# Kernel tuning notes

Hardware: AMD Instinct MI355X
Metric: run time of the kernel (lower is better)

The kernel has to match this reference:

```python
import jax, jax.numpy as jnp
import numpy as np
from jax import lax

B, NR, NT, M, NUM_ITER = 16384, 64, 32, 4, 64


def setup_inputs() -> dict:
    key = jax.random.key(0)
    k1, k2, k3 = jax.random.split(key, 3)
    yt = jax.random.normal(k1, (B, NR), dtype=jnp.float32)
    # scale channel to keep the 64-step unrolled descent numerically stable
    Ht = 0.1 * jax.random.normal(k2, (B, NR, NT), dtype=jnp.float32)
    sigmat0 = 0.5 + 0.5 * jax.random.uniform(k3, (B,), dtype=jnp.float32)
    m = jnp.array([-3.0, -1.0, 1.0, 3.0], dtype=jnp.float32)          # 4-PAM constellation
    alpha = jnp.full((M,), 0.25, dtype=jnp.float32)                    # uniform prior
    taui = jnp.ones((NUM_ITER + 1,), dtype=jnp.float32)                # taui0 = 1
    delta = jnp.full((NUM_ITER,), 0.1, dtype=jnp.float32)              # delta0 = 0.1
    return {"yt": yt, "Ht": Ht, "sigmat0": sigmat0, "m": m, "alpha": alpha,
            "taui": taui, "delta": delta}


def reference(yt, Ht, sigmat0, m, alpha, taui, delta):
    # Precompute as in CMDNet.call
    HH = jnp.einsum('bri,brj->bij', Ht, Ht)          # [B, Nt, Nt] = H^T H
    yH = jnp.einsum('br,brj->bj', yt, Ht)            # [B, Nt]     = y^T H
    Bsz, _, Nt = Ht.shape
    Mc = m.shape[0]
    n_iter = delta.shape[0]

    G0 = jnp.zeros((Bsz, Nt, Mc), dtype=Ht.dtype)
    sig2 = (sigmat0 ** 2)[:, None, None]             # [B,1,1]
    log_alpha = jnp.log(alpha)                       # [M]
    taui_abs = jnp.abs(taui)                         # [num_iter+1]
    # first layer uses scale 1 in the softmax (first_iter=True), but taui_abs in grad_x
    ft_scale = taui_abs[:n_iter].at[0].set(1.0)

    def step(G, inp):
        scale, ta, d = inp
        ft = jax.nn.softmax((log_alpha + G) * scale, axis=-1)   # [B,Nt,M]
        xt = jnp.sum(ft * m, axis=-1)                           # [B,Nt] soft symbol
        xHH = jnp.einsum('bi,bij->bj', xt, HH)                  # [B,Nt]
        grad_x = ta * (ft * m - ft * xt[..., None])             # [B,Nt,M]
        grad_L = sig2 * (1.0 - jnp.exp(-G)) + grad_x * (xHH - yH)[..., None]
        return G - d * grad_L, None

    G, _ = lax.scan(step, G0, (ft_scale, taui_abs[:n_iter], delta))

    # last layer (last_iter=True): softmax + soft symbol only, no update
    ft = jax.nn.softmax((log_alpha + G) * taui_abs[n_iter], axis=-1)
    xt = jnp.sum(ft * m, axis=-1)
    return ft, xt
```

## Files before the change

kernel.cpp:

```cpp
#include <hip/hip_runtime.h>


#define NRr 64
#define NTt 32
#define NITER 64
#define B_TOTAL 16384

using f16x8  = __attribute__((ext_vector_type(8))) _Float16;
using h16x2  = __attribute__((ext_vector_type(2))) _Float16;
using f32x16 = __attribute__((ext_vector_type(16))) float;

static __device__ __forceinline__ uint32_t pk16(float a, float b) {
    union { _Float16 h[2]; uint32_t u; } x;
    x.h[0] = (_Float16)a; x.h[1] = (_Float16)b;
    return x.u;
}

static __device__ __forceinline__ float fdot2u(uint32_t a, uint32_t b, float c) {
    union { uint32_t u; h16x2 h; } x, y;
    x.u = a; y.u = b;
#if __has_builtin(__builtin_amdgcn_fdot2)
    return __builtin_amdgcn_fdot2(x.h, y.h, c, false);
#else
    return c + (float)x.h[0] * (float)y.h[0] + (float)x.h[1] * (float)y.h[1];
#endif
}

static __device__ __forceinline__ float exp2fast(float x) {
#if __has_builtin(__builtin_amdgcn_exp2f)
    return __builtin_amdgcn_exp2f(x);
#else
    return exp2f(x);
#endif
}

static __device__ __forceinline__ float rdlane(float v, int lane) {
    return __builtin_bit_cast(float,
        __builtin_amdgcn_readlane(__builtin_bit_cast(int, v), lane));
}

static __device__ __forceinline__ float rfl(float v) {
    return __builtin_bit_cast(float,
        __builtin_amdgcn_readfirstlane(__builtin_bit_cast(int, v)));
}

static __device__ __forceinline__ void gram_one(
    const float* __restrict__ hp, const float* __restrict__ ypt,
    const int hi, uint32_t ap[8], float& ypart_out)
{
    f32x16 acc = {};
    float  ypart = 0.f;
#pragma unroll
    for (int kc = 0; kc < 4; ++kc) {
        const int kb = kc * 16 + hi * 8;
        float h[8];
#pragma unroll
        for (int e = 0; e < 8; ++e) h[e] = hp[(size_t)(kb + e) * NTt];
        const float4 ya = *(const float4*)(ypt + kb);
        const float4 yb = *(const float4*)(ypt + kb + 4);
        ypart += h[0]*ya.x + h[1]*ya.y + h[2]*ya.z + h[3]*ya.w
               + h[4]*yb.x + h[5]*yb.y + h[6]*yb.z + h[7]*yb.w;
        f16x8 fa;
#pragma unroll
        for (int e = 0; e < 8; ++e) fa[e] = (_Float16)h[e];
        acc = __builtin_amdgcn_mfma_f32_32x32x16_f16(fa, fa, acc, 0, 0, 0);
    }
#pragma unroll
    for (int g = 0; g < 4; ++g) {
        ap[2*g+0] = pk16(acc[4*g+0], acc[4*g+1]);
        ap[2*g+1] = pk16(acc[4*g+2], acc[4*g+3]);
    }
    ypart_out = ypart;
}

static __device__ __forceinline__ void exch_hh(
    const uint32_t apx[8], const uint32_t apy[8], const int hi, uint32_t hh[16])
{
#pragma unroll
    for (int p = 0; p < 8; ++p) {
        const uint32_t snd = hi ? apx[p] : apy[p];
        const uint32_t rcv = (uint32_t)__shfl_xor((int)snd, 32, 64);
        const uint32_t own = hi ? apy[p] : apx[p];
        const int g = p >> 1, cc = p & 1;
        hh[4*g + cc]     = hi ? rcv : own;
        hh[4*g + 2 + cc] = hi ? own : rcv;
    }
}

__global__ __launch_bounds__(256)
__attribute__((amdgpu_waves_per_eu(4, 4)))
void cmdnet_kernel(
    const float* __restrict__ yt,
    const float* __restrict__ Ht,
    const float* __restrict__ sig0,
    const float* __restrict__ mm,
    const float* __restrict__ alpha,
    const float* __restrict__ taui,
    const float* __restrict__ delta,
    float* __restrict__ out)
{
    __shared__ __align__(16) _Float16 xtsh[4][4][32];

    const int tid = threadIdx.x;
    const int w   = tid >> 6;
    const int l   = tid & 63;
    const int j   = l & 31;
    const int hi  = l >> 5;
    const int c0  = (blockIdx.x * 4 + w) * 4;

    const float vta = fabsf(taui[l]);
    const float vd  = delta[l];

    const size_t hstride = (size_t)NRr * NTt;

    uint32_t hhA[16], hhB[16];
    float yHA_v, yHB_v;
    {
        uint32_t apx[8], apy[8];
        float ypx, ypy;
        gram_one(Ht + (size_t)(c0    ) * hstride + j, yt + (size_t)(c0    ) * NRr, hi, apx, ypx);
        gram_one(Ht + (size_t)(c0 + 2) * hstride + j, yt + (size_t)(c0 + 2) * NRr, hi, apy, ypy);
        exch_hh(apx, apy, hi, hhA);
        const float snd = hi ? ypx : ypy;
        const float rcv = __shfl_xor(snd, 32, 64);
        yHA_v = (hi ? ypy : ypx) + rcv;
    }
    {
        uint32_t apx[8], apy[8];
        float ypx, ypy;
        gram_one(Ht + (size_t)(c0 + 1) * hstride + j, yt + (size_t)(c0 + 1) * NRr, hi, apx, ypx);
        gram_one(Ht + (size_t)(c0 + 3) * hstride + j, yt + (size_t)(c0 + 3) * NRr, hi, apy, ypy);
        exch_hh(apx, apy, hi, hhB);
        const float snd = hi ? ypx : ypy;
        const float rcv = __shfl_xor(snd, 32, 64);
        yHB_v = (hi ? ypy : ypx) + rcv;
    }

    const int bA = c0 + 2*hi;
    const int bB = bA + 1;
    const float sgA = sig0[bA], sgB = sig0[bB];
    const float sig2A = sgA * sgA, sig2B = sgB * sgB;

    const float4 mv = *(const float4*)mm;
    const float4 av = *(const float4*)alpha;
    const float m0 = rfl(mv.x), m1 = rfl(mv.y), m2 = rfl(mv.z), m3 = rfl(mv.w);
    const float la0 = rfl(__log2f(av.x)), la1 = rfl(__log2f(av.y));
    const float la2 = rfl(__log2f(av.z)), la3 = rfl(__log2f(av.w));

    const float L2E  = 1.4426950408889634f;
    const float NL2E = -1.4426950408889634f;

    _Float16* xwA = &xtsh[w][2*hi][j];
    _Float16* xwB = &xtsh[w][2*hi+1][j];
    const uint4* xr = (const uint4*)&xtsh[w][2*hi][0];

    float GA0 = 0.f, GA1 = 0.f, GA2 = 0.f, GA3 = 0.f;
    float GB0 = 0.f, GB1 = 0.f, GB2 = 0.f, GB3 = 0.f;

    for (int it = 0; it < NITER; ++it) {
        const float ta  = rdlane(vta, it);
        const float d   = rdlane(vd,  it);
        const float sc  = (it == 0) ? 1.0f : ta;
        const float scL = sc * L2E;
        const float tad = ta * d;
        const float c1A = d * sig2A, c1B = d * sig2B;
        const float ls0 = la0 * sc, ls1 = la1 * sc,
                    ls2 = la2 * sc, ls3 = la3 * sc;

        const float sA0 = fmaf(GA0, scL, ls0), sA1 = fmaf(GA1, scL, ls1);
        const float sA2 = fmaf(GA2, scL, ls2), sA3 = fmaf(GA3, scL, ls3);
        const float sB0 = fmaf(GB0, scL, ls0), sB1 = fmaf(GB1, scL, ls1);
        const float sB2 = fmaf(GB2, scL, ls2), sB3 = fmaf(GB3, scL, ls3);
        const float mxA = fmaxf(fmaxf(sA0, sA1), fmaxf(sA2, sA3));
        const float mxB = fmaxf(fmaxf(sB0, sB1), fmaxf(sB2, sB3));
        const float eA0 = exp2fast(sA0 - mxA), eA1 = exp2fast(sA1 - mxA);
        const float eA2 = exp2fast(sA2 - mxA), eA3 = exp2fast(sA3 - mxA);
        const float eB0 = exp2fast(sB0 - mxB), eB1 = exp2fast(sB1 - mxB);
        const float eB2 = exp2fast(sB2 - mxB), eB3 = exp2fast(sB3 - mxB);
        const float ZA = (eA0 + eA1) + (eA2 + eA3);
        const float ZB = (eB0 + eB1) + (eB2 + eB3);
        const float RA = __builtin_amdgcn_rcpf(ZA);
        const float RB = __builtin_amdgcn_rcpf(ZB);
        const float SA = fmaf(eA0, m0, fmaf(eA1, m1, fmaf(eA2, m2, eA3 * m3)));
        const float SB = fmaf(eB0, m0, fmaf(eB1, m1, fmaf(eB2, m2, eB3 * m3)));
        const float xtA = SA * RA;
        const float xtB = SB * RB;

        *xwA = (_Float16)xtA;
        *xwB = (_Float16)xtB;
        asm volatile("" ::: "memory");

        const float enA0 = exp2fast(GA0 * NL2E), enA1 = exp2fast(GA1 * NL2E);
        const float enA2 = exp2fast(GA2 * NL2E), enA3 = exp2fast(GA3 * NL2E);
        const float enB0 = exp2fast(GB0 * NL2E), enB1 = exp2fast(GB1 * NL2E);
        const float enB2 = exp2fast(GB2 * NL2E), enB3 = exp2fast(GB3 * NL2E);

        const uint4 a0 = xr[0], a1 = xr[1], a2 = xr[2], a3 = xr[3];
        const uint4 b0 = xr[4], b1 = xr[5], b2 = xr[6], b3 = xr[7];
        asm volatile("" ::: "memory");

        float pA0 = 0.f, pA1 = 0.f, pB0 = 0.f, pB1 = 0.f;
        pA0 = fdot2u(hhA[ 0], a0.x, pA0); pA1 = fdot2u(hhA[ 1], a0.y, pA1);
        pB0 = fdot2u(hhB[ 0], b0.x, pB0); pB1 = fdot2u(hhB[ 1], b0.y, pB1);
        pA0 = fdot2u(hhA[ 2], a0.z, pA0); pA1 = fdot2u(hhA[ 3], a0.w, pA1);
        pB0 = fdot2u(hhB[ 2], b0.z, pB0); pB1 = fdot2u(hhB[ 3], b0.w, pB1);
        pA0 = fdot2u(hhA[ 4], a1.x, pA0); pA1 = fdot2u(hhA[ 5], a1.y, pA1);
        pB0 = fdot2u(hhB[ 4], b1.x, pB0); pB1 = fdot2u(hhB[ 5], b1.y, pB1);
        pA0 = fdot2u(hhA[ 6], a1.z, pA0); pA1 = fdot2u(hhA[ 7], a1.w, pA1);
        pB0 = fdot2u(hhB[ 6], b1.z, pB0); pB1 = fdot2u(hhB[ 7], b1.w, pB1);
        pA0 = fdot2u(hhA[ 8], a2.x, pA0); pA1 = fdot2u(hhA[ 9], a2.y, pA1);
        pB0 = fdot2u(hhB[ 8], b2.x, pB0); pB1 = fdot2u(hhB[ 9], b2.y, pB1);
        pA0 = fdot2u(hhA[10], a2.z, pA0); pA1 = fdot2u(hhA[11], a2.w, pA1);
        pB0 = fdot2u(hhB[10], b2.z, pB0); pB1 = fdot2u(hhB[11], b2.w, pB1);
        pA0 = fdot2u(hhA[12], a3.x, pA0); pA1 = fdot2u(hhA[13], a3.y, pA1);
        pB0 = fdot2u(hhB[12], b3.x, pB0); pB1 = fdot2u(hhB[13], b3.y, pB1);
        pA0 = fdot2u(hhA[14], a3.z, pA0); pA1 = fdot2u(hhA[15], a3.w, pA1);
        pB0 = fdot2u(hhB[14], b3.z, pB0); pB1 = fdot2u(hhB[15], b3.w, pB1);

        const float qdA = (pA0 + pA1) - yHA_v;
        const float qdB = (pB0 + pB1) - yHB_v;
        const float tqA = tad * qdA * RA;
        const float tqB = tad * qdB * RB;

        GA0 = fmaf(-tqA, eA0 * (m0 - xtA), fmaf(c1A, enA0, GA0 - c1A));
        GA1 = fmaf(-tqA, eA1 * (m1 - xtA), fmaf(c1A, enA1, GA1 - c1A));
        GA2 = fmaf(-tqA, eA2 * (m2 - xtA), fmaf(c1A, enA2, GA2 - c1A));
        GA3 = fmaf(-tqA, eA3 * (m3 - xtA), fmaf(c1A, enA3, GA3 - c1A));
        GB0 = fmaf(-tqB, eB0 * (m0 - xtB), fmaf(c1B, enB0, GB0 - c1B));
        GB1 = fmaf(-tqB, eB1 * (m1 - xtB), fmaf(c1B, enB1, GB1 - c1B));
        GB2 = fmaf(-tqB, eB2 * (m2 - xtB), fmaf(c1B, enB2, GB2 - c1B));
        GB3 = fmaf(-tqB, eB3 * (m3 - xtB), fmaf(c1B, enB3, GB3 - c1B));
    }

    const float tap = fabsf(taui[NITER]);
#pragma unroll
    for (int s = 0; s < 2; ++s) {
        const float G0 = s ? GB0 : GA0, G1 = s ? GB1 : GA1;
        const float G2 = s ? GB2 : GA2, G3 = s ? GB3 : GA3;
        const int   bm = s ? bB : bA;
        const float w0 = fmaf(G0, L2E, la0) * tap;
        const float w1 = fmaf(G1, L2E, la1) * tap;
        const float w2 = fmaf(G2, L2E, la2) * tap;
        const float w3 = fmaf(G3, L2E, la3) * tap;
        const float mx = fmaxf(fmaxf(w0, w1), fmaxf(w2, w3));
        const float e0 = exp2fast(w0 - mx), e1 = exp2fast(w1 - mx);
        const float e2 = exp2fast(w2 - mx), e3 = exp2fast(w3 - mx);
        const float Z  = (e0 + e1) + (e2 + e3);
        const float R  = __builtin_amdgcn_rcpf(Z);
        const float f0 = e0 * R, f1 = e1 * R, f2 = e2 * R, f3 = e3 * R;
        const float xt = fmaf(f0, m0, fmaf(f1, m1, fmaf(f2, m2, f3 * m3)));

        float4 f4; f4.x = f0; f4.y = f1; f4.z = f2; f4.w = f3;
        *(float4*)(out + ((size_t)bm * NTt + j) * 4) = f4;
        out[(size_t)B_TOTAL * NTt * 4 + (size_t)bm * NTt + j] = xt;
    }
}

extern "C" void kernel_launch(void* const* d_in, const int* in_sizes, int n_in,
                              void* d_out, int out_size, void* d_ws, size_t ws_size,
                              hipStream_t stream) {
    const float* yt    = (const float*)d_in[0];
    const float* Ht    = (const float*)d_in[1];
    const float* sig0  = (const float*)d_in[2];
    const float* mm    = (const float*)d_in[3];
    const float* alpha = (const float*)d_in[4];
    const float* taui  = (const float*)d_in[5];
    const float* delta = (const float*)d_in[6];
    float* out = (float*)d_out;

    const int blocks = B_TOTAL / 16;
    cmdnet_kernel<<<blocks, 256, 0, stream>>>(yt, Ht, sig0, mm, alpha, taui,
                                              delta, out);
}
```

Measured before the change: 95.53 us.

## Process two batch items per wave instead of four, doubling occupancy

```diff
diff --git a/kernel.cpp b/kernel.cpp
--- a/kernel.cpp
+++ b/kernel.cpp
@@ -88,7 +88,7 @@
 }
 
 __global__ __launch_bounds__(256)
-__attribute__((amdgpu_waves_per_eu(4, 4)))
+__attribute__((amdgpu_waves_per_eu(8, 8)))
 void cmdnet_kernel(
     const float* __restrict__ yt,
     const float* __restrict__ Ht,
@@ -99,47 +99,36 @@
     const float* __restrict__ delta,
     float* __restrict__ out)
 {
-    __shared__ __align__(16) _Float16 xtsh[4][4][32];
+    __shared__ __align__(16) _Float16 xtsh[4][2][32];
 
     const int tid = threadIdx.x;
     const int w   = tid >> 6;
     const int l   = tid & 63;
     const int j   = l & 31;
     const int hi  = l >> 5;
-    const int c0  = (blockIdx.x * 4 + w) * 4;
+    const int c0  = (blockIdx.x * 4 + w) * 2;
 
     const float vta = fabsf(taui[l]);
     const float vd  = delta[l];
 
     const size_t hstride = (size_t)NRr * NTt;
 
-    uint32_t hhA[16], hhB[16];
-    float yHA_v, yHB_v;
+    uint32_t hh[16];
+    float yH_v;
     {
         uint32_t apx[8], apy[8];
         float ypx, ypy;
         gram_one(Ht + (size_t)(c0    ) * hstride + j, yt + (size_t)(c0    ) * NRr, hi, apx, ypx);
-        gram_one(Ht + (size_t)(c0 + 2) * hstride + j, yt + (size_t)(c0 + 2) * NRr, hi, apy, ypy);
-        exch_hh(apx, apy, hi, hhA);
+        gram_one(Ht + (size_t)(c0 + 1) * hstride + j, yt + (size_t)(c0 + 1) * NRr, hi, apy, ypy);
+        exch_hh(apx, apy, hi, hh);
         const float snd = hi ? ypx : ypy;
         const float rcv = __shfl_xor(snd, 32, 64);
-        yHA_v = (hi ? ypy : ypx) + rcv;
-    }
-    {
-        uint32_t apx[8], apy[8];
-        float ypx, ypy;
-        gram_one(Ht + (size_t)(c0 + 1) * hstride + j, yt + (size_t)(c0 + 1) * NRr, hi, apx, ypx);
-        gram_one(Ht + (size_t)(c0 + 3) * hstride + j, yt + (size_t)(c0 + 3) * NRr, hi, apy, ypy);
-        exch_hh(apx, apy, hi, hhB);
-        const float snd = hi ? ypx : ypy;
-        const float rcv = __shfl_xor(snd, 32, 64);
-        yHB_v = (hi ? ypy : ypx) + rcv;
-    }
-
-    const int bA = c0 + 2*hi;
-    const int bB = bA + 1;
-    const float sgA = sig0[bA], sgB = sig0[bB];
-    const float sig2A = sgA * sgA, sig2B = sgB * sgB;
+        yH_v = (hi ? ypy : ypx) + rcv;
+    }
+
+    const int   bmy  = c0 + hi;
+    const float sgv  = sig0[bmy];
+    const float sig2 = sgv * sgv;
 
     const float4 mv = *(const float4*)mm;
     const float4 av = *(const float4*)alpha;
@@ -150,12 +139,10 @@
     const float L2E  = 1.4426950408889634f;
     const float NL2E = -1.4426950408889634f;
 
-    _Float16* xwA = &xtsh[w][2*hi][j];
-    _Float16* xwB = &xtsh[w][2*hi+1][j];
-    const uint4* xr = (const uint4*)&xtsh[w][2*hi][0];
-
-    float GA0 = 0.f, GA1 = 0.f, GA2 = 0.f, GA3 = 0.f;
-    float GB0 = 0.f, GB1 = 0.f, GB2 = 0.f, GB3 = 0.f;
+    _Float16*    xwp = &xtsh[w][hi][j];
+    const uint4* xrp = (const uint4*)&xtsh[w][hi][0];
+
+    float G0 = 0.f, G1 = 0.f, G2 = 0.f, G3 = 0.f;
 
     for (int it = 0; it < NITER; ++it) {
         const float ta  = rdlane(vta, it);
@@ -163,81 +150,50 @@
         const float sc  = (it == 0) ? 1.0f : ta;
         const float scL = sc * L2E;
         const float tad = ta * d;
-        const float c1A = d * sig2A, c1B = d * sig2B;
+        const float c1  = d * sig2;
         const float ls0 = la0 * sc, ls1 = la1 * sc,
                     ls2 = la2 * sc, ls3 = la3 * sc;
 
-        const float sA0 = fmaf(GA0, scL, ls0), sA1 = fmaf(GA1, scL, ls1);
-        const float sA2 = fmaf(GA2, scL, ls2), sA3 = fmaf(GA3, scL, ls3);
-        const float sB0 = fmaf(GB0, scL, ls0), sB1 = fmaf(GB1, scL, ls1);
-        const float sB2 = fmaf(GB2, scL, ls2), sB3 = fmaf(GB3, scL, ls3);
-        const float mxA = fmaxf(fmaxf(sA0, sA1), fmaxf(sA2, sA3));
-        const float mxB = fmaxf(fmaxf(sB0, sB1), fmaxf(sB2, sB3));
-        const float eA0 = exp2fast(sA0 - mxA), eA1 = exp2fast(sA1 - mxA);
-        const float eA2 = exp2fast(sA2 - mxA), eA3 = exp2fast(sA3 - mxA);
-        const float eB0 = exp2fast(sB0 - mxB), eB1 = exp2fast(sB1 - mxB);
-        const float eB2 = exp2fast(sB2 - mxB), eB3 = exp2fast(sB3 - mxB);
-        const float ZA = (eA0 + eA1) + (eA2 + eA3);
-        const float ZB = (eB0 + eB1) + (eB2 + eB3);
-        const float RA = __builtin_amdgcn_rcpf(ZA);
-        const float RB = __builtin_amdgcn_rcpf(ZB);
-        const float SA = fmaf(eA0, m0, fmaf(eA1, m1, fmaf(eA2, m2, eA3 * m3)));
-        const float SB = fmaf(eB0, m0, fmaf(eB1, m1, fmaf(eB2, m2, eB3 * m3)));
-        const float xtA = SA * RA;
-        const float xtB = SB * RB;
-
-        *xwA = (_Float16)xtA;
-        *xwB = (_Float16)xtB;
+        const float s0 = fmaf(G0, scL, ls0), s1 = fmaf(G1, scL, ls1);
+        const float s2 = fmaf(G2, scL, ls2), s3 = fmaf(G3, scL, ls3);
+        const float mx = fmaxf(fmaxf(s0, s1), fmaxf(s2, s3));
+        const float e0 = exp2fast(s0 - mx), e1 = exp2fast(s1 - mx);
+        const float e2 = exp2fast(s2 - mx), e3 = exp2fast(s3 - mx);
+        const float Z  = (e0 + e1) + (e2 + e3);
+        const float R  = __builtin_amdgcn_rcpf(Z);
+        const float S  = fmaf(e0, m0, fmaf(e1, m1, fmaf(e2, m2, e3 * m3)));
+        const float xt = S * R;
+
+        *xwp = (_Float16)xt;
         asm volatile("" ::: "memory");
 
-        const float enA0 = exp2fast(GA0 * NL2E), enA1 = exp2fast(GA1 * NL2E);
-        const float enA2 = exp2fast(GA2 * NL2E), enA3 = exp2fast(GA3 * NL2E);
-        const float enB0 = exp2fast(GB0 * NL2E), enB1 = exp2fast(GB1 * NL2E);
-        const float enB2 = exp2fast(GB2 * NL2E), enB3 = exp2fast(GB3 * NL2E);
-
-        const uint4 a0 = xr[0], a1 = xr[1], a2 = xr[2], a3 = xr[3];
-        const uint4 b0 = xr[4], b1 = xr[5], b2 = xr[6], b3 = xr[7];
+        const float en0 = exp2fast(G0 * NL2E), en1 = exp2fast(G1 * NL2E);
+        const float en2 = exp2fast(G2 * NL2E), en3 = exp2fast(G3 * NL2E);
+
+        const uint4 a0 = xrp[0], a1 = xrp[1], a2 = xrp[2], a3 = xrp[3];
         asm volatile("" ::: "memory");
 
-        float pA0 = 0.f, pA1 = 0.f, pB0 = 0.f, pB1 = 0.f;
-        pA0 = fdot2u(hhA[ 0], a0.x, pA0); pA1 = fdot2u(hhA[ 1], a0.y, pA1);
-        pB0 = fdot2u(hhB[ 0], b0.x, pB0); pB1 = fdot2u(hhB[ 1], b0.y, pB1);
-        pA0 = fdot2u(hhA[ 2], a0.z, pA0); pA1 = fdot2u(hhA[ 3], a0.w, pA1);
-        pB0 = fdot2u(hhB[ 2], b0.z, pB0); pB1 = fdot2u(hhB[ 3], b0.w, pB1);
-        pA0 = fdot2u(hhA[ 4], a1.x, pA0); pA1 = fdot2u(hhA[ 5], a1.y, pA1);
-        pB0 = fdot2u(hhB[ 4], b1.x, pB0); pB1 = fdot2u(hhB[ 5], b1.y, pB1);
-        pA0 = fdot2u(hhA[ 6], a1.z, pA0); pA1 = fdot2u(hhA[ 7], a1.w, pA1);
-        pB0 = fdot2u(hhB[ 6], b1.z, pB0); pB1 = fdot2u(hhB[ 7], b1.w, pB1);
-        pA0 = fdot2u(hhA[ 8], a2.x, pA0); pA1 = fdot2u(hhA[ 9], a2.y, pA1);
-        pB0 = fdot2u(hhB[ 8], b2.x, pB0); pB1 = fdot2u(hhB[ 9], b2.y, pB1);
-        pA0 = fdot2u(hhA[10], a2.z, pA0); pA1 = fdot2u(hhA[11], a2.w, pA1);
-        pB0 = fdot2u(hhB[10], b2.z, pB0); pB1 = fdot2u(hhB[11], b2.w, pB1);
-        pA0 = fdot2u(hhA[12], a3.x, pA0); pA1 = fdot2u(hhA[13], a3.y, pA1);
-        pB0 = fdot2u(hhB[12], b3.x, pB0); pB1 = fdot2u(hhB[13], b3.y, pB1);
-        pA0 = fdot2u(hhA[14], a3.z, pA0); pA1 = fdot2u(hhA[15], a3.w, pA1);
-        pB0 = fdot2u(hhB[14], b3.z, pB0); pB1 = fdot2u(hhB[15], b3.w, pB1);
-
-        const float qdA = (pA0 + pA1) - yHA_v;
-        const float qdB = (pB0 + pB1) - yHB_v;
-        const float tqA = tad * qdA * RA;
-        const float tqB = tad * qdB * RB;
-
-        GA0 = fmaf(-tqA, eA0 * (m0 - xtA), fmaf(c1A, enA0, GA0 - c1A));
-        GA1 = fmaf(-tqA, eA1 * (m1 - xtA), fmaf(c1A, enA1, GA1 - c1A));
-        GA2 = fmaf(-tqA, eA2 * (m2 - xtA), fmaf(c1A, enA2, GA2 - c1A));
-        GA3 = fmaf(-tqA, eA3 * (m3 - xtA), fmaf(c1A, enA3, GA3 - c1A));
-        GB0 = fmaf(-tqB, eB0 * (m0 - xtB), fmaf(c1B, enB0, GB0 - c1B));
-        GB1 = fmaf(-tqB, eB1 * (m1 - xtB), fmaf(c1B, enB1, GB1 - c1B));
-        GB2 = fmaf(-tqB, eB2 * (m2 - xtB), fmaf(c1B, enB2, GB2 - c1B));
-        GB3 = fmaf(-tqB, eB3 * (m3 - xtB), fmaf(c1B, enB3, GB3 - c1B));
+        float p0 = 0.f, p1 = 0.f;
+        p0 = fdot2u(hh[ 0], a0.x, p0); p1 = fdot2u(hh[ 1], a0.y, p1);
+        p0 = fdot2u(hh[ 2], a0.z, p0); p1 = fdot2u(hh[ 3], a0.w, p1);
+        p0 = fdot2u(hh[ 4], a1.x, p0); p1 = fdot2u(hh[ 5], a1.y, p1);
+        p0 = fdot2u(hh[ 6], a1.z, p0); p1 = fdot2u(hh[ 7], a1.w, p1);
+        p0 = fdot2u(hh[ 8], a2.x, p0); p1 = fdot2u(hh[ 9], a2.y, p1);
+        p0 = fdot2u(hh[10], a2.z, p0); p1 = fdot2u(hh[11], a2.w, p1);
+        p0 = fdot2u(hh[12], a3.x, p0); p1 = fdot2u(hh[13], a3.y, p1);
+        p0 = fdot2u(hh[14], a3.z, p0); p1 = fdot2u(hh[15], a3.w, p1);
+
+        const float qd = (p0 + p1) - yH_v;
+        const float tq = tad * qd * R;
+
+        G0 = fmaf(-tq, e0 * (m0 - xt), fmaf(c1, en0, G0 - c1));
+        G1 = fmaf(-tq, e1 * (m1 - xt), fmaf(c1, en1, G1 - c1));
+        G2 = fmaf(-tq, e2 * (m2 - xt), fmaf(c1, en2, G2 - c1));
+        G3 = fmaf(-tq, e3 * (m3 - xt), fmaf(c1, en3, G3 - c1));
     }
 
     const float tap = fabsf(taui[NITER]);
-#pragma unroll
-    for (int s = 0; s < 2; ++s) {
-        const float G0 = s ? GB0 : GA0, G1 = s ? GB1 : GA1;
-        const float G2 = s ? GB2 : GA2, G3 = s ? GB3 : GA3;
-        const int   bm = s ? bB : bA;
+    {
         const float w0 = fmaf(G0, L2E, la0) * tap;
         const float w1 = fmaf(G1, L2E, la1) * tap;
         const float w2 = fmaf(G2, L2E, la2) * tap;
@@ -251,8 +207,8 @@
         const float xt = fmaf(f0, m0, fmaf(f1, m1, fmaf(f2, m2, f3 * m3)));
 
         float4 f4; f4.x = f0; f4.y = f1; f4.z = f2; f4.w = f3;
-        *(float4*)(out + ((size_t)bm * NTt + j) * 4) = f4;
-        out[(size_t)B_TOTAL * NTt * 4 + (size_t)bm * NTt + j] = xt;
+        *(float4*)(out + ((size_t)bmy * NTt + j) * 4) = f4;
+        out[(size_t)B_TOTAL * NTt * 4 + (size_t)bmy * NTt + j] = xt;
     }
 }
 
@@ -268,7 +224,7 @@
     const float* delta = (const float*)d_in[6];
     float* out = (float*)d_out;
 
-    const int blocks = B_TOTAL / 16;
+    const int blocks = B_TOTAL / 8;
     cmdnet_kernel<<<blocks, 256, 0, stream>>>(yt, Ht, sig0, mm, alpha, taui,
                                               delta, out);
 }
```

After: 118.1 us. 23.7% more time.

## Compute per-iteration xt·HH matvec with MFMA instead of fdot2 chains

Applied to the files above, without the earlier changes.

```diff
diff --git a/kernel.cpp b/kernel.cpp
--- a/kernel.cpp
+++ b/kernel.cpp
@@ -7,7 +7,7 @@
 #define B_TOTAL 16384
 
 using f16x8  = __attribute__((ext_vector_type(8))) _Float16;
-using h16x2  = __attribute__((ext_vector_type(2))) _Float16;
+using u32x4  = __attribute__((ext_vector_type(4))) unsigned int;
 using f32x16 = __attribute__((ext_vector_type(16))) float;
 
 static __device__ __forceinline__ uint32_t pk16(float a, float b) {
@@ -16,14 +16,10 @@
     return x.u;
 }
 
-static __device__ __forceinline__ float fdot2u(uint32_t a, uint32_t b, float c) {
-    union { uint32_t u; h16x2 h; } x, y;
-    x.u = a; y.u = b;
-#if __has_builtin(__builtin_amdgcn_fdot2)
-    return __builtin_amdgcn_fdot2(x.h, y.h, c, false);
-#else
-    return c + (float)x.h[0] * (float)y.h[0] + (float)x.h[1] * (float)y.h[1];
-#endif
+static __device__ __forceinline__ f16x8 mk8(uint32_t a, uint32_t b,
+                                            uint32_t c, uint32_t d) {
+    u32x4 t; t[0] = a; t[1] = b; t[2] = c; t[3] = d;
+    return __builtin_bit_cast(f16x8, t);
 }
 
 static __device__ __forceinline__ float exp2fast(float x) {
@@ -44,6 +40,10 @@
         __builtin_amdgcn_readfirstlane(__builtin_bit_cast(int, v)));
 }
 
+static __device__ __forceinline__ uint32_t shflx32(uint32_t v) {
+    return (uint32_t)__shfl_xor((int)v, 32, 64);
+}
+
 static __device__ __forceinline__ void gram_one(
     const float* __restrict__ hp, const float* __restrict__ ypt,
     const int hi, uint32_t ap[8], float& ypart_out)
@@ -71,20 +71,6 @@
         ap[2*g+1] = pk16(acc[4*g+2], acc[4*g+3]);
     }
     ypart_out = ypart;
-}
-
-static __device__ __forceinline__ void exch_hh(
-    const uint32_t apx[8], const uint32_t apy[8], const int hi, uint32_t hh[16])
-{
-#pragma unroll
-    for (int p = 0; p < 8; ++p) {
-        const uint32_t snd = hi ? apx[p] : apy[p];
-        const uint32_t rcv = (uint32_t)__shfl_xor((int)snd, 32, 64);
-        const uint32_t own = hi ? apy[p] : apx[p];
-        const int g = p >> 1, cc = p & 1;
-        hh[4*g + cc]     = hi ? rcv : own;
-        hh[4*g + 2 + cc] = hi ? own : rcv;
-    }
 }
 
 __global__ __launch_bounds__(256)
@@ -113,28 +99,24 @@
 
     const size_t hstride = (size_t)NRr * NTt;
 
-    uint32_t hhA[16], hhB[16];
-    float yHA_v, yHB_v;
-    {
-        uint32_t apx[8], apy[8];
-        float ypx, ypy;
-        gram_one(Ht + (size_t)(c0    ) * hstride + j, yt + (size_t)(c0    ) * NRr, hi, apx, ypx);
-        gram_one(Ht + (size_t)(c0 + 2) * hstride + j, yt + (size_t)(c0 + 2) * NRr, hi, apy, ypy);
-        exch_hh(apx, apy, hi, hhA);
-        const float snd = hi ? ypx : ypy;
-        const float rcv = __shfl_xor(snd, 32, 64);
-        yHA_v = (hi ? ypy : ypx) + rcv;
-    }
-    {
-        uint32_t apx[8], apy[8];
-        float ypx, ypy;
-        gram_one(Ht + (size_t)(c0 + 1) * hstride + j, yt + (size_t)(c0 + 1) * NRr, hi, apx, ypx);
-        gram_one(Ht + (size_t)(c0 + 3) * hstride + j, yt + (size_t)(c0 + 3) * NRr, hi, apy, ypy);
-        exch_hh(apx, apy, hi, hhB);
-        const float snd = hi ? ypx : ypy;
-        const float rcv = __shfl_xor(snd, 32, 64);
-        yHB_v = (hi ? ypy : ypx) + rcv;
-    }
+    f16x8 bff[4][2];
+    float ysum[4];
+#pragma unroll
+    for (int c = 0; c < 4; ++c) {
+        uint32_t ap[8];
+        float yp;
+        gram_one(Ht + (size_t)(c0 + c) * hstride + j,
+                 yt + (size_t)(c0 + c) * NRr, hi, ap, yp);
+        const uint32_t r0 = shflx32(hi ? ap[0] : ap[2]);
+        const uint32_t r1 = shflx32(hi ? ap[1] : ap[3]);
+        const uint32_t r2 = shflx32(hi ? ap[4] : ap[6]);
+        const uint32_t r3 = shflx32(hi ? ap[5] : ap[7]);
+        bff[c][0] = hi ? mk8(r0, r1, ap[2], ap[3]) : mk8(ap[0], ap[1], r0, r1);
+        bff[c][1] = hi ? mk8(r2, r3, ap[6], ap[7]) : mk8(ap[4], ap[5], r2, r3);
+        ysum[c] = yp + __shfl_xor(yp, 32, 64);
+    }
+    const float yHA_v = hi ? ysum[2] : ysum[0];
+    const float yHB_v = hi ? ysum[3] : ysum[1];
 
     const int bA = c0 + 2*hi;
     const int bB = bA + 1;
@@ -152,7 +134,10 @@
 
     _Float16* xwA = &xtsh[w][2*hi][j];
     _Float16* xwB = &xtsh[w][2*hi+1][j];
-    const uint4* xr = (const uint4*)&xtsh[w][2*hi][0];
+    const u32x4* xs = (const u32x4*)&xtsh[w][0][0];
+    const int afb = hi;
+
+    const f32x16 zc = {};
 
     float GA0 = 0.f, GA1 = 0.f, GA2 = 0.f, GA3 = 0.f;
     float GB0 = 0.f, GB1 = 0.f, GB2 = 0.f, GB3 = 0.f;
@@ -171,8 +156,8 @@
         const float sA2 = fmaf(GA2, scL, ls2), sA3 = fmaf(GA3, scL, ls3);
         const float sB0 = fmaf(GB0, scL, ls0), sB1 = fmaf(GB1, scL, ls1);
         const float sB2 = fmaf(GB2, scL, ls2), sB3 = fmaf(GB3, scL, ls3);
-        const float mxA = fmaxf(fmaxf(sA0, sA1), fmaxf(sA2, sA3));
-        const float mxB = fmaxf(fmaxf(sB0, sB1), fmaxf(sB2, sB3));
+        const float mxA = fmaxf(fmaxf(fmaxf(sA0, sA1), sA2), sA3);
+        const float mxB = fmaxf(fmaxf(fmaxf(sB0, sB1), sB2), sB3);
         const float eA0 = exp2fast(sA0 - mxA), eA1 = exp2fast(sA1 - mxA);
         const float eA2 = exp2fast(sA2 - mxA), eA3 = exp2fast(sA3 - mxA);
         const float eB0 = exp2fast(sB0 - mxB), eB1 = exp2fast(sB1 - mxB);
@@ -195,30 +180,24 @@
         const float enB0 = exp2fast(GB0 * NL2E), enB1 = exp2fast(GB1 * NL2E);
         const float enB2 = exp2fast(GB2 * NL2E), enB3 = exp2fast(GB3 * NL2E);
 
-        const uint4 a0 = xr[0], a1 = xr[1], a2 = xr[2], a3 = xr[3];
-        const uint4 b0 = xr[4], b1 = xr[5], b2 = xr[6], b3 = xr[7];
+        float xh[4];
+#pragma unroll
+        for (int c = 0; c < 4; ++c) {
+            const f16x8 a0 = __builtin_bit_cast(f16x8, xs[c*4 + 0*2 + afb]);
+            const f16x8 a1 = __builtin_bit_cast(f16x8, xs[c*4 + 1*2 + afb]);
+            f32x16 acc = __builtin_amdgcn_mfma_f32_32x32x16_f16(
+                             a0, bff[c][0], zc, 0, 0, 0);
+            acc = __builtin_amdgcn_mfma_f32_32x32x16_f16(
+                             a1, bff[c][1], acc, 0, 0, 0);
+            xh[c] = acc[0];
+        }
         asm volatile("" ::: "memory");
 
-        float pA0 = 0.f, pA1 = 0.f, pB0 = 0.f, pB1 = 0.f;
-        pA0 = fdot2u(hhA[ 0], a0.x, pA0); pA1 = fdot2u(hhA[ 1], a0.y, pA1);
-        pB0 = fdot2u(hhB[ 0], b0.x, pB0); pB1 = fdot2u(hhB[ 1], b0.y, pB1);
-        pA0 = fdot2u(hhA[ 2], a0.z, pA0); pA1 = fdot2u(hhA[ 3], a0.w, pA1);
-        pB0 = fdot2u(hhB[ 2], b0.z, pB0); pB1 = fdot2u(hhB[ 3], b0.w, pB1);
-        pA0 = fdot2u(hhA[ 4], a1.x, pA0); pA1 = fdot2u(hhA[ 5], a1.y, pA1);
-        pB0 = fdot2u(hhB[ 4], b1.x, pB0); pB1 = fdot2u(hhB[ 5], b1.y, pB1);
-        pA0 = fdot2u(hhA[ 6], a1.z, pA0); pA1 = fdot2u(hhA[ 7], a1.w, pA1);
-        pB0 = fdot2u(hhB[ 6], b1.z, pB0); pB1 = fdot2u(hhB[ 7], b1.w, pB1);
-        pA0 = fdot2u(hhA[ 8], a2.x, pA0); pA1 = fdot2u(hhA[ 9], a2.y, pA1);
-        pB0 = fdot2u(hhB[ 8], b2.x, pB0); pB1 = fdot2u(hhB[ 9], b2.y, pB1);
-        pA0 = fdot2u(hhA[10], a2.z, pA0); pA1 = fdot2u(hhA[11], a2.w, pA1);
-        pB0 = fdot2u(hhB[10], b2.z, pB0); pB1 = fdot2u(hhB[11], b2.w, pB1);
-        pA0 = fdot2u(hhA[12], a3.x, pA0); pA1 = fdot2u(hhA[13], a3.y, pA1);
-        pB0 = fdot2u(hhB[12], b3.x, pB0); pB1 = fdot2u(hhB[13], b3.y, pB1);
-        pA0 = fdot2u(hhA[14], a3.z, pA0); pA1 = fdot2u(hhA[15], a3.w, pA1);
-        pB0 = fdot2u(hhB[14], b3.z, pB0); pB1 = fdot2u(hhB[15], b3.w, pB1);
-
-        const float qdA = (pA0 + pA1) - yHA_v;
-        const float qdB = (pB0 + pB1) - yHB_v;
+        const float pA = hi ? xh[2] : xh[0];
+        const float pB = hi ? xh[3] : xh[1];
+
+        const float qdA = pA - yHA_v;
+        const float qdB = pB - yHB_v;
         const float tqA = tad * qdA * RA;
         const float tqB = tad * qdB * RB;
 
@@ -242,7 +221,7 @@
         const float w1 = fmaf(G1, L2E, la1) * tap;
         const float w2 = fmaf(G2, L2E, la2) * tap;
         const float w3 = fmaf(G3, L2E, la3) * tap;
-        const float mx = fmaxf(fmaxf(w0, w1), fmaxf(w2, w3));
+        const float mx = fmaxf(fmaxf(fmaxf(w0, w1), w2), w3);
         const float e0 = exp2fast(w0 - mx), e1 = exp2fast(w1 - mx);
         const float e2 = exp2fast(w2 - mx), e3 = exp2fast(w3 - mx);
         const float Z  = (e0 + e1) + (e2 + e3);
```

Result: slower. 106.2 us (+11.2%).
